# Performance work log

Measured on AMD Instinct MI355X. Metric: run time of the kernel, lower is better.

## Reference

```python
import jax, jax.numpy as jnp
import numpy as np

MARGIN = 2.0


def setup_inputs() -> dict:
    key = jax.random.key(0)
    k1, k2 = jax.random.split(key)
    predict = jax.random.normal(k1, (8192, 2048, 1, 1), dtype=jnp.float32)
    gt = jax.random.randint(k2, (8192, 1), 0, 751, dtype=jnp.int64)
    return {"predict": predict, "gt": gt}


def reference(predict, gt):
    # predict: [B, 2048, 1, 1] -> [B, D]
    p = predict.reshape(predict.shape[0], -1)
    b, d = p.shape
    # pairwise squared L2 distance / dim, via GEMM (||a||^2 + ||b||^2 - 2 a.b)
    sq = jnp.sum(p * p, axis=1)  # [B]
    d2 = (sq[:, None] + sq[None, :] - 2.0 * (p @ p.T))
    d2 = jnp.maximum(d2, 0.0) / d  # clamp tiny negatives from GEMM roundoff
    g = gt.reshape(-1)
    label = (g[:, None] == g[None, :]).astype(p.dtype)  # [B, B]
    term = label * d2 + (1.0 - label) * jax.nn.relu(MARGIN - d2)
    # original loop sums over j >= i (diagonal contributes 0: same label, dist 0)
    mask = jnp.triu(jnp.ones((b, b), dtype=bool))
    loss = jnp.sum(jnp.where(mask, term, 0.0))
    return 2.0 * loss / (b * (b - 1))
```

## Files before the change

kernel.cpp:

```cpp
#include <hip/hip_runtime.h>
#include <stdint.h>

#define NROWS 8192
#define DIM   2048
#define MARGIN 2.0f
#define SCALEQ (127.0f / 6.0f)
#define S2     ((6.0f / 127.0f) * (6.0f / 127.0f))

#define BT2     256
#define BKB     128
#define NKT     (DIM / BKB)
#define NT2     (NROWS / BT2)
#define NTILES2 (NT2 * (NT2 + 1) / 2)
#define NQ      16
#define ABUF_B  32768
#define BUF_B   65536
#define HALF_B  16384

typedef __attribute__((ext_vector_type(4)))  int  int4v;
typedef __attribute__((ext_vector_type(16))) int  int16v;
typedef unsigned char uchar;

__device__ __forceinline__ void decode_tile(int bid, int* ti, int* tj) {
    float fn = (float)NT2 + 0.5f;
    int r = (int)(fn - sqrtf(fn * fn - 2.0f * (float)bid));
    if (r < 0) r = 0;
    if (r >= NT2) r = NT2 - 1;
    while ((r + 1) * NT2 - ((r + 1) * r) / 2 <= bid) ++r;
    while (r * NT2 - (r * (r - 1)) / 2 > bid) --r;
    *ti = r;
    *tj = r + (bid - (r * NT2 - (r * (r - 1)) / 2));
}

__device__ __forceinline__ uint pack4(float4 v) {
    int q0 = (int)__builtin_rintf(v.x * SCALEQ);
    int q1 = (int)__builtin_rintf(v.y * SCALEQ);
    int q2 = (int)__builtin_rintf(v.z * SCALEQ);
    int q3 = (int)__builtin_rintf(v.w * SCALEQ);
    q0 = min(max(q0, -127), 127); q1 = min(max(q1, -127), 127);
    q2 = min(max(q2, -127), 127); q3 = min(max(q3, -127), 127);
    return (uint)(q0 & 0xFF) | ((uint)(q1 & 0xFF) << 8) |
           ((uint)(q2 & 0xFF) << 16) | ((uint)(q3 & 0xFF) << 24);
}

__global__ __launch_bounds__(256) void prep_kernel(const float* __restrict__ p,
                                                   uchar* __restrict__ pb,
                                                   float* __restrict__ sq) {
    int row = blockIdx.x;
    int t = threadIdx.x;
    const float4* prow = (const float4*)(p + (size_t)row * DIM);
    uint* qrow = (uint*)(pb + (size_t)row * DIM);
    float4 a = prow[t];
    float4 b = prow[t + 256];
    float s = a.x * a.x + a.y * a.y + a.z * a.z + a.w * a.w
            + b.x * b.x + b.y * b.y + b.z * b.z + b.w * b.w;
    qrow[t] = pack4(a);
    qrow[t + 256] = pack4(b);
#pragma unroll
    for (int o = 32; o > 0; o >>= 1) s += __shfl_down(s, o, 64);
    __shared__ float wsums[4];
    int lane = t & 63, wvv = t >> 6;
    if (lane == 0) wsums[wvv] = s;
    __syncthreads();
    if (t == 0) sq[row] = wsums[0] + wsums[1] + wsums[2] + wsums[3];
}

__device__ __forceinline__ void stage_ht(const uchar* __restrict__ pb,
                                         uchar* lds, int t, int which,
                                         int ibase, int jbase, int tid) {
    if (t >= NKT) t -= 2;
    const int h = which & 1;
    const int row0 = ((which >= 2) ? jbase : ibase) + h * 128;
    const uchar* g0 = pb + (size_t)row0 * DIM + t * BKB;
    uchar* l0 = lds + (t & 1) * BUF_B + ((which >= 2) ? ABUF_B : 0) + h * HALF_B;
#pragma unroll
    for (int r = 0; r < 2; ++r) {
        int row = r * 64 + (tid >> 3);
        int c8 = (tid & 7) ^ ((tid >> 3) & 7);
        const uchar* g = g0 + (size_t)row * DIM + c8 * 16;
        uchar* l = l0 + r * 8192 + (tid >> 6) * 1024;
        __builtin_amdgcn_global_load_lds(
            (const __attribute__((address_space(1))) uint32_t*)g,
            (__attribute__((address_space(3))) uint32_t*)l, 16, 0, 0);
    }
}

__device__ __forceinline__ void stage_qA(const uchar* __restrict__ pb,
                                         uchar* lds, int t, int ibase, int tid) {
    if (t >= NKT) t -= 2;
    const uchar* g0 = pb + (size_t)ibase * DIM + t * BKB;
    uchar* l0 = lds + (t & 1) * BUF_B;
    int row = tid >> 3;
    int c8 = (tid & 7) ^ ((tid >> 3) & 7);
    const uchar* g = g0 + (size_t)row * DIM + c8 * 16;
    uchar* l = l0 + (tid >> 6) * 1024;
    __builtin_amdgcn_global_load_lds(
        (const __attribute__((address_space(1))) uint32_t*)g,
        (__attribute__((address_space(3))) uint32_t*)l, 16, 0, 0);
}

#define BARF()   do { __builtin_amdgcn_s_barrier(); \
                      asm volatile("" ::: "memory"); } while (0)
#define WAITL()  asm volatile("s_waitcnt lgkmcnt(0)" ::: "memory")
#define WAITV8() asm volatile("s_waitcnt vmcnt(8)" ::: "memory")
#define WAITV5() asm volatile("s_waitcnt vmcnt(5)" ::: "memory")
#define WAITV0() asm volatile("s_waitcnt vmcnt(0)" ::: "memory")
#define PRIO1()  __builtin_amdgcn_s_setprio(1)
#define PRIO0()  __builtin_amdgcn_s_setprio(0)

#define READ_A(AB, MH)                                                         \
    _Pragma("unroll") for (int mt = 0; mt < 2; ++mt)                           \
    _Pragma("unroll") for (int s = 0; s < 4; ++s) {                            \
        int rl = wr * 128 + ((MH) * 2 + mt) * 32 + (lane & 31);                \
        af[mt][s] = *(const int4v*)&(AB)[rl * 128 +                            \
                     (((2 * s + kh) ^ (lane & 7)) * 16)];                      \
    }

#define READ_B(BB, NH)                                                         \
    _Pragma("unroll") for (int s = 0; s < 4; ++s) {                            \
        int rl = wc * 64 + (NH) * 32 + (lane & 31);                            \
        bf[NH][s] = *(const int4v*)&(BB)[rl * 128 +                            \
                     (((2 * s + kh) ^ (lane & 7)) * 16)];                      \
    }

#define MFMA_Q(MH, NH)                                                         \
    _Pragma("unroll") for (int mt = 0; mt < 2; ++mt)                           \
    _Pragma("unroll") for (int s = 0; s < 4; ++s)                              \
        acc[(MH) * 2 + mt][NH] = __builtin_amdgcn_mfma_i32_32x32x32_i8(        \
            af[mt][s], bf[NH][s], acc[(MH) * 2 + mt][NH], 0, 0, 0);

#define STEP_FULL(T, BUF)                                                      \
    {                                                                          \
        const uchar* Ab = &lds[(BUF) * BUF_B];                                 \
        const uchar* Bb = &lds[(BUF) * BUF_B + ABUF_B];                        \
                                       \
        READ_A(Ab, 0);                                                         \
        READ_B(Bb, 0);                                                         \
        BARF(); WAITL();                                                       \
        PRIO1(); MFMA_Q(0, 0); PRIO0();                                        \
        BARF();                                                                \
                                                  \
        READ_B(Bb, 1);                                                         \
        BARF(); WAITL();                                                       \
        PRIO1(); MFMA_Q(0, 1); PRIO0();                                        \
        BARF();                                                                \
                                   \
        READ_A(Ab, 1);                                                         \
        stage_ht(pb, lds, (T) + 2, 2, ibase, jbase, tid);                      \
        stage_ht(pb, lds, (T) + 2, 3, ibase, jbase, tid);                      \
        BARF(); WAITL();                                                       \
        PRIO1(); MFMA_Q(1, 0); PRIO0();                                        \
        BARF();                                                                \
                \
        stage_ht(pb, lds, (T) + 2, 0, ibase, jbase, tid);                      \
        stage_ht(pb, lds, (T) + 2, 1, ibase, jbase, tid);                      \
        PRIO1(); MFMA_Q(1, 1); PRIO0();                                        \
        WAITV8(); BARF();                                                      \
    }

#define STEP_Q(T, BUF)                                                         \
    {                                                                          \
        const uchar* Ab = &lds[(BUF) * BUF_B];                                 \
        const uchar* Bb = &lds[(BUF) * BUF_B + ABUF_B];                        \
        _Pragma("unroll") for (int mt = 0; mt < 2; ++mt)                       \
        _Pragma("unroll") for (int s = 0; s < 4; ++s) {                        \
            int rl = mt * 32 + (lane & 31);                                    \
            aq[mt][s] = *(const int4v*)&Ab[rl * 128 +                          \
                         (((2 * s + kh) ^ (lane & 7)) * 16)];                  \
        }                                                                      \
        _Pragma("unroll") for (int s = 0; s < 4; ++s) {                        \
            int rl = wv * 32 + (lane & 31);                                    \
            bq[s] = *(const int4v*)&Bb[rl * 128 +                              \
                     (((2 * s + kh) ^ (lane & 7)) * 16)];                      \
        }                                                                      \
        WAITL();                                                               \
        PRIO1();                                                               \
        _Pragma("unroll") for (int s = 0; s < 4; ++s)                          \
        _Pragma("unroll") for (int mt = 0; mt < 2; ++mt)                       \
            accq[mt] = __builtin_amdgcn_mfma_i32_32x32x32_i8(                  \
                aq[mt][s], bq[s], accq[mt], 0, 0, 0);                          \
        PRIO0();                                                               \
        BARF();                                                                \
        stage_qA(pb, lds, (T) + 2, ibase, tid);                                \
        stage_ht(pb, lds, (T) + 2, 2, ibase, jbase, tid);                      \
        stage_ht(pb, lds, (T) + 2, 3, ibase, jbase, tid);                      \
        WAITV5(); BARF();                                                      \
    }

__global__ __launch_bounds__(512) void tile2_kernel(
    const uchar* __restrict__ pb, const float* __restrict__ sq,
    const int* __restrict__ gt, double* __restrict__ accum) {

    __shared__ uchar lds[2 * BUF_B];
    __shared__ float wsum[8];

    const int bx = (int)blockIdx.x;
    const bool is_q = (bx < 4 * NQ);
    int bid, qq = 0;
    if (is_q) { bid = bx >> 2; qq = bx & 3; }
    else { int f = bx - 4 * NQ; bid = NQ + ((f & 7) << 6) + (f >> 3); }

    int ti, tj;
    decode_tile(bid, &ti, &tj);

    const int tid = threadIdx.x;
    const int lane = tid & 63;
    const int kh = lane >> 5;
    const int wv = tid >> 6;
    const int wr = wv >> 2;
    const int wc = wv & 3;
    const int jbase = tj * BT2;
    const int ibase = ti * BT2 + (is_q ? qq * 64 : 0);

    const float invd = 1.0f / (float)DIM;
    float lsum = 0.f;

    if (!is_q) {
        int16v acc[4][2] = {};
        int4v af[2][4];
        int4v bf[2][4];

        stage_ht(pb, lds, 0, 2, ibase, jbase, tid);
        stage_ht(pb, lds, 0, 3, ibase, jbase, tid);
        stage_ht(pb, lds, 0, 0, ibase, jbase, tid);
        stage_ht(pb, lds, 0, 1, ibase, jbase, tid);
        stage_ht(pb, lds, 1, 2, ibase, jbase, tid);
        stage_ht(pb, lds, 1, 3, ibase, jbase, tid);
        stage_ht(pb, lds, 1, 0, ibase, jbase, tid);
        stage_ht(pb, lds, 1, 1, ibase, jbase, tid);
        WAITV8();
        BARF();

#pragma unroll 1
        for (int s0 = 0; s0 < NKT; s0 += 2) {
            STEP_FULL(s0, 0);
            STEP_FULL(s0 + 1, 1);
        }
        WAITV0();
        BARF();

        int j0 = jbase + wc * 64 + (lane & 31);
        float sqj[2]; int gj[2];
#pragma unroll
        for (int n = 0; n < 2; ++n) { int j = j0 + n * 32; sqj[n] = sq[j]; gj[n] = gt[j]; }
        const float wb = (ti != tj) ? 2.0f : 1.0f;
#pragma unroll
        for (int mi = 0; mi < 4; ++mi) {
#pragma unroll
            for (int q = 0; q < 4; ++q) {
#pragma unroll
                for (int rr = 0; rr < 4; ++rr) {
                    int i = ibase + wr * 128 + mi * 32 + rr + 8 * q + 4 * kh;
                    float sqi = sq[i];
                    int gi = gt[i];
#pragma unroll
                    for (int n = 0; n < 2; ++n) {
                        int j = j0 + n * 32;
                        float dot = S2 * (float)acc[mi][n][q * 4 + rr];
                        float d2 = fmaxf(sqi + sqj[n] - 2.0f * dot, 0.0f) * invd;
                        float term = (gi == gj[n]) ? d2 : fmaxf(MARGIN - d2, 0.0f);
                        float w = wb;
                        if (ti == tj && i == j) w = 2.0f;
                        lsum += w * term;
                    }
                }
            }
        }
    } else {
        int16v accq[2] = {};
        int4v aq[2][4], bq[4];

        stage_qA(pb, lds, 0, ibase, tid);
        stage_ht(pb, lds, 0, 2, ibase, jbase, tid);
        stage_ht(pb, lds, 0, 3, ibase, jbase, tid);
        stage_qA(pb, lds, 1, ibase, tid);
        stage_ht(pb, lds, 1, 2, ibase, jbase, tid);
        stage_ht(pb, lds, 1, 3, ibase, jbase, tid);
        WAITV5();
        BARF();

#pragma unroll 1
        for (int s0 = 0; s0 < NKT; s0 += 2) {
            STEP_Q(s0, 0);
            STEP_Q(s0 + 1, 1);
        }
        WAITV0();
        BARF();

        int j = jbase + wv * 32 + (lane & 31);
        float sqj = sq[j];
        int gj = gt[j];
        const float wb = (ti != tj) ? 2.0f : 1.0f;
#pragma unroll
        for (int mt = 0; mt < 2; ++mt) {
#pragma unroll
            for (int q = 0; q < 4; ++q) {
#pragma unroll
                for (int rr = 0; rr < 4; ++rr) {
                    int i = ibase + mt * 32 + rr + 8 * q + 4 * kh;
                    float dot = S2 * (float)accq[mt][q * 4 + rr];
                    float d2 = fmaxf(sq[i] + sqj - 2.0f * dot, 0.0f) * invd;
                    float term = (gt[i] == gj) ? d2 : fmaxf(MARGIN - d2, 0.0f);
                    float w = wb;
                    if (ti == tj && i == j) w = 2.0f;
                    lsum += w * term;
                }
            }
        }
    }

#pragma unroll
    for (int o = 32; o > 0; o >>= 1) lsum += __shfl_down(lsum, o, 64);
    if (lane == 0) wsum[wv] = lsum;
    __syncthreads();
    if (tid == 0) {
        float s = 0.f;
#pragma unroll
        for (int w = 0; w < 8; ++w) s += wsum[w];
        atomicAdd(accum, (double)s);
    }
}

__global__ void finalize_kernel(const double* __restrict__ accum,
                                float* __restrict__ out) {
    if (threadIdx.x == 0)
        out[0] = (float)(accum[0] * (1.0 / ((double)NROWS * (double)(NROWS - 1))));
}

extern "C" void kernel_launch(void* const* d_in, const int* in_sizes, int n_in,
                              void* d_out, int out_size, void* d_ws, size_t ws_size,
                              hipStream_t stream) {
    (void)in_sizes; (void)n_in; (void)out_size; (void)ws_size;
    const float* p = (const float*)d_in[0];
    const int* gt = (const int*)d_in[1];
    float* out = (float*)d_out;

    uchar* pb = (uchar*)d_ws;
    size_t off = (size_t)NROWS * DIM;
    float* sq = (float*)((char*)d_ws + off);
    off += (size_t)NROWS * sizeof(float);
    double* accum = (double*)((char*)d_ws + off);

    (void)hipMemsetAsync(accum, 0, sizeof(double), stream);
    prep_kernel<<<NROWS, 256, 0, stream>>>(p, pb, sq);
    tile2_kernel<<<4 * NQ + 512, 512, 0, stream>>>(pb, sq, gt, accum);
    finalize_kernel<<<1, 64, 0, stream>>>(accum, out);
}
```

Baseline: 114.3 us.

## Switch int8 GEMM tile pipeline from double-buffered LDS to single buffer

Replaces the two-stage LDS double buffer (128 KB) with a single 64 KB buffer. Each K-step now reads all fragments into registers, hits a barrier, issues the next tile's global-to-LDS loads, then runs the remaining MFMAs while those loads are in flight, ending with a full vmcnt(0) wait. The smaller LDS footprint could let two workgroups share a CU and simplifies the per-step barrier sequence. The cost is that the prefetch distance drops from two tiles to one, so load latency is exposed whenever the second half of the MFMAs is too short to cover it.

After: 122.6 us. +7.3%, slower.

```diff
diff --git a/kernel.cpp b/kernel.cpp
--- a/kernel.cpp
+++ b/kernel.cpp
@@ -13,9 +13,7 @@
 #define NT2     (NROWS / BT2)
 #define NTILES2 (NT2 * (NT2 + 1) / 2)
 #define NQ      16
-#define ABUF_B  32768
-#define BUF_B   65536
-#define HALF_B  16384
+#define BOFF    32768
 
 typedef __attribute__((ext_vector_type(4)))  int  int4v;
 typedef __attribute__((ext_vector_type(16))) int  int16v;
@@ -68,11 +66,11 @@
 __device__ __forceinline__ void stage_ht(const uchar* __restrict__ pb,
                                          uchar* lds, int t, int which,
                                          int ibase, int jbase, int tid) {
-    if (t >= NKT) t -= 2;
+    if (t >= NKT) t = NKT - 1;
     const int h = which & 1;
     const int row0 = ((which >= 2) ? jbase : ibase) + h * 128;
     const uchar* g0 = pb + (size_t)row0 * DIM + t * BKB;
-    uchar* l0 = lds + (t & 1) * BUF_B + ((which >= 2) ? ABUF_B : 0) + h * HALF_B;
+    uchar* l0 = lds + ((which >= 2) ? BOFF : 0) + h * 16384;
 #pragma unroll
     for (int r = 0; r < 2; ++r) {
         int row = r * 64 + (tid >> 3);
@@ -87,13 +85,12 @@
 
 __device__ __forceinline__ void stage_qA(const uchar* __restrict__ pb,
                                          uchar* lds, int t, int ibase, int tid) {
-    if (t >= NKT) t -= 2;
+    if (t >= NKT) t = NKT - 1;
     const uchar* g0 = pb + (size_t)ibase * DIM + t * BKB;
-    uchar* l0 = lds + (t & 1) * BUF_B;
     int row = tid >> 3;
     int c8 = (tid & 7) ^ ((tid >> 3) & 7);
     const uchar* g = g0 + (size_t)row * DIM + c8 * 16;
-    uchar* l = l0 + (tid >> 6) * 1024;
+    uchar* l = lds + (tid >> 6) * 1024;
     __builtin_amdgcn_global_load_lds(
         (const __attribute__((address_space(1))) uint32_t*)g,
         (__attribute__((address_space(3))) uint32_t*)l, 16, 0, 0);
@@ -102,24 +99,23 @@
 #define BARF()   do { __builtin_amdgcn_s_barrier(); \
                       asm volatile("" ::: "memory"); } while (0)
 #define WAITL()  asm volatile("s_waitcnt lgkmcnt(0)" ::: "memory")
-#define WAITV8() asm volatile("s_waitcnt vmcnt(8)" ::: "memory")
-#define WAITV5() asm volatile("s_waitcnt vmcnt(5)" ::: "memory")
 #define WAITV0() asm volatile("s_waitcnt vmcnt(0)" ::: "memory")
 #define PRIO1()  __builtin_amdgcn_s_setprio(1)
 #define PRIO0()  __builtin_amdgcn_s_setprio(0)
-
-#define READ_A(AB, MH)                                                         \
+#define SB0()    __builtin_amdgcn_sched_barrier(0)
+
+#define READ_A(MH)                                                             \
     _Pragma("unroll") for (int mt = 0; mt < 2; ++mt)                           \
     _Pragma("unroll") for (int s = 0; s < 4; ++s) {                            \
         int rl = wr * 128 + ((MH) * 2 + mt) * 32 + (lane & 31);                \
-        af[mt][s] = *(const int4v*)&(AB)[rl * 128 +                            \
+        af[mt][s] = *(const int4v*)&lds[rl * 128 +                             \
                      (((2 * s + kh) ^ (lane & 7)) * 16)];                      \
     }
 
-#define READ_B(BB, NH)                                                         \
+#define READ_B(NH)                                                             \
     _Pragma("unroll") for (int s = 0; s < 4; ++s) {                            \
         int rl = wc * 64 + (NH) * 32 + (lane & 31);                            \
-        bf[NH][s] = *(const int4v*)&(BB)[rl * 128 +                            \
+        bf[NH][s] = *(const int4v*)&lds[BOFF + rl * 128 +                      \
                      (((2 * s + kh) ^ (lane & 7)) * 16)];                      \
     }
 
@@ -129,69 +125,55 @@
         acc[(MH) * 2 + mt][NH] = __builtin_amdgcn_mfma_i32_32x32x32_i8(        \
             af[mt][s], bf[NH][s], acc[(MH) * 2 + mt][NH], 0, 0, 0);
 
-#define STEP_FULL(T, BUF)                                                      \
+#define STEP_FULL(T)                                                           \
     {                                                                          \
-        const uchar* Ab = &lds[(BUF) * BUF_B];                                 \
-        const uchar* Bb = &lds[(BUF) * BUF_B + ABUF_B];                        \
-                                       \
-        READ_A(Ab, 0);                                                         \
-        READ_B(Bb, 0);                                                         \
-        BARF(); WAITL();                                                       \
-        PRIO1(); MFMA_Q(0, 0); PRIO0();                                        \
-        BARF();                                                                \
-                                                  \
-        READ_B(Bb, 1);                                                         \
-        BARF(); WAITL();                                                       \
-        PRIO1(); MFMA_Q(0, 1); PRIO0();                                        \
-        BARF();                                                                \
-                                   \
-        READ_A(Ab, 1);                                                         \
-        stage_ht(pb, lds, (T) + 2, 2, ibase, jbase, tid);                      \
-        stage_ht(pb, lds, (T) + 2, 3, ibase, jbase, tid);                      \
-        BARF(); WAITL();                                                       \
-        PRIO1(); MFMA_Q(1, 0); PRIO0();                                        \
-        BARF();                                                                \
-                \
-        stage_ht(pb, lds, (T) + 2, 0, ibase, jbase, tid);                      \
-        stage_ht(pb, lds, (T) + 2, 1, ibase, jbase, tid);                      \
-        PRIO1(); MFMA_Q(1, 1); PRIO0();                                        \
-        WAITV8(); BARF();                                                      \
-    }
-
-#define STEP_Q(T, BUF)                                                         \
+        READ_A(0);                                                             \
+        READ_B(0);                                                             \
+        READ_B(1);                                                             \
+        PRIO1(); MFMA_Q(0, 0); MFMA_Q(0, 1); PRIO0();                          \
+        READ_A(1);                                                             \
+        WAITL(); BARF();                                                       \
+        stage_ht(pb, lds, (T) + 1, 2, ibase, jbase, tid);                      \
+        stage_ht(pb, lds, (T) + 1, 3, ibase, jbase, tid);                      \
+        stage_ht(pb, lds, (T) + 1, 0, ibase, jbase, tid);                      \
+        stage_ht(pb, lds, (T) + 1, 1, ibase, jbase, tid);                      \
+        SB0();                                                                 \
+        PRIO1(); MFMA_Q(1, 0); MFMA_Q(1, 1); PRIO0();                          \
+        WAITV0(); BARF();                                                      \
+    }
+
+#define STEP_Q(T)                                                              \
     {                                                                          \
-        const uchar* Ab = &lds[(BUF) * BUF_B];                                 \
-        const uchar* Bb = &lds[(BUF) * BUF_B + ABUF_B];                        \
         _Pragma("unroll") for (int mt = 0; mt < 2; ++mt)                       \
         _Pragma("unroll") for (int s = 0; s < 4; ++s) {                        \
             int rl = mt * 32 + (lane & 31);                                    \
-            aq[mt][s] = *(const int4v*)&Ab[rl * 128 +                          \
+            aq[mt][s] = *(const int4v*)&lds[rl * 128 +                         \
                          (((2 * s + kh) ^ (lane & 7)) * 16)];                  \
         }                                                                      \
         _Pragma("unroll") for (int s = 0; s < 4; ++s) {                        \
             int rl = wv * 32 + (lane & 31);                                    \
-            bq[s] = *(const int4v*)&Bb[rl * 128 +                              \
+            bq[s] = *(const int4v*)&lds[BOFF + rl * 128 +                      \
                      (((2 * s + kh) ^ (lane & 7)) * 16)];                      \
         }                                                                      \
-        WAITL();                                                               \
+        WAITL(); BARF();                                                       \
+        stage_qA(pb, lds, (T) + 1, ibase, tid);                                \
+        stage_ht(pb, lds, (T) + 1, 2, ibase, jbase, tid);                      \
+        stage_ht(pb, lds, (T) + 1, 3, ibase, jbase, tid);                      \
+        SB0();                                                                 \
         PRIO1();                                                               \
         _Pragma("unroll") for (int s = 0; s < 4; ++s)                          \
         _Pragma("unroll") for (int mt = 0; mt < 2; ++mt)                       \
             accq[mt] = __builtin_amdgcn_mfma_i32_32x32x32_i8(                  \
                 aq[mt][s], bq[s], accq[mt], 0, 0, 0);                          \
         PRIO0();                                                               \
-        BARF();                                                                \
-        stage_qA(pb, lds, (T) + 2, ibase, tid);                                \
-        stage_ht(pb, lds, (T) + 2, 2, ibase, jbase, tid);                      \
-        stage_ht(pb, lds, (T) + 2, 3, ibase, jbase, tid);                      \
-        WAITV5(); BARF();                                                      \
+        WAITV0(); BARF();                                                      \
     }
 
 __global__ __launch_bounds__(512) void tile2_kernel(
     const uchar* __restrict__ pb, const float* __restrict__ sq,
     const int* __restrict__ gt, double* __restrict__ accum) {
 
-    __shared__ uchar lds[2 * BUF_B];
+    __shared__ uchar lds[65536];
     __shared__ float wsum[8];
 
     const int bx = (int)blockIdx.x;
@@ -224,20 +206,13 @@
         stage_ht(pb, lds, 0, 3, ibase, jbase, tid);
         stage_ht(pb, lds, 0, 0, ibase, jbase, tid);
         stage_ht(pb, lds, 0, 1, ibase, jbase, tid);
-        stage_ht(pb, lds, 1, 2, ibase, jbase, tid);
-        stage_ht(pb, lds, 1, 3, ibase, jbase, tid);
-        stage_ht(pb, lds, 1, 0, ibase, jbase, tid);
-        stage_ht(pb, lds, 1, 1, ibase, jbase, tid);
-        WAITV8();
-        BARF();
-
-#pragma unroll 1
-        for (int s0 = 0; s0 < NKT; s0 += 2) {
-            STEP_FULL(s0, 0);
-            STEP_FULL(s0 + 1, 1);
-        }
         WAITV0();
         BARF();
+
+#pragma unroll 1
+        for (int s0 = 0; s0 < NKT; ++s0) {
+            STEP_FULL(s0);
+        }
 
         int j0 = jbase + wc * 64 + (lane & 31);
         float sqj[2]; int gj[2];
@@ -273,19 +248,13 @@
         stage_qA(pb, lds, 0, ibase, tid);
         stage_ht(pb, lds, 0, 2, ibase, jbase, tid);
         stage_ht(pb, lds, 0, 3, ibase, jbase, tid);
-        stage_qA(pb, lds, 1, ibase, tid);
-        stage_ht(pb, lds, 1, 2, ibase, jbase, tid);
-        stage_ht(pb, lds, 1, 3, ibase, jbase, tid);
-        WAITV5();
-        BARF();
-
-#pragma unroll 1
-        for (int s0 = 0; s0 < NKT; s0 += 2) {
-            STEP_Q(s0, 0);
-            STEP_Q(s0 + 1, 1);
-        }
         WAITV0();
         BARF();
+
+#pragma unroll 1
+        for (int s0 = 0; s0 < NKT; ++s0) {
+            STEP_Q(s0);
+        }
 
         int j = jbase + wv * 32 + (lane & 31);
         float sqj = sq[j];
```
